# Performance work log

Measured on AMD Instinct MI355X. Metric: run time of the kernel, lower is better.

Reference implementation:

```python
import jax, jax.numpy as jnp
import numpy as np

B = 50000        # mini-batch nodes
NB, M, D = 4, 256, 32   # branches, codebook size, per-branch dim
C = NB * D       # in_channels = out_channels = 128
E = 1000000      # edges per block (intra and cross)
N_GLOBAL = 100000


def setup_inputs() -> dict:
    key = jax.random.key(0)
    ks = jax.random.split(key, 16)
    return {
        "X_B": jax.random.normal(ks[0], (B, C), dtype=jnp.float32),
        "edge_src_bb": jax.random.randint(ks[1], (E,), 0, B),
        "edge_dst_bb": jax.random.randint(ks[2], (E,), 0, B),
        "edge_w_bb": jax.random.uniform(ks[3], (E,), dtype=jnp.float32),
        "edge_src_bm": jax.random.randint(ks[4], (E,), 0, N_GLOBAL),
        "edge_dst_bm": jax.random.randint(ks[5], (E,), 0, B),
        "edge_w_bm": jax.random.uniform(ks[6], (E,), dtype=jnp.float32),
        "c_indices": jax.random.randint(ks[7], (N_GLOBAL,), 0, M),
        "warm_up_rate": jnp.ones((1,), dtype=jnp.float32),
        "codebook": jax.random.normal(ks[8], (NB, M, D), dtype=jnp.float32),
        "vq_grad": jax.random.normal(ks[9], (NB, M, D), dtype=jnp.float32) * 0.01,
        "W_conv": jax.random.normal(ks[10], (NB, D, D), dtype=jnp.float32) / np.sqrt(D),
        "b_conv": jax.random.normal(ks[11], (NB, D), dtype=jnp.float32) * 0.01,
        "W_fc": jax.random.normal(ks[12], (C, C), dtype=jnp.float32) / np.sqrt(C),
        "b_fc": jax.random.normal(ks[13], (C,), dtype=jnp.float32) * 0.01,
    }


def reference(X_B, edge_src_bb, edge_dst_bb, edge_w_bb, edge_src_bm, edge_dst_bm,
              edge_w_bm, c_indices, warm_up_rate, codebook, vq_grad,
              W_conv, b_conv, W_fc, b_fc):
    wr = warm_up_rate[0]
    # split features into NB branches: [NB, B, D]
    Xb = X_B.reshape(B, NB, D).transpose(1, 0, 2)
    # X_input = cat([X_B, codebook * warm_up_rate]) per branch -> [NB, B+M, D]
    X_in = jnp.concatenate([Xb, codebook * wr], axis=1)
    # GCNConv (normalize=False): linear transform then edge-weighted aggregation
    h = jnp.einsum('nbd,nde->nbe', X_in, W_conv)
    # mapper: remap out-of-batch endpoints of cross edges to codeword rows
    src_bm = B + c_indices[edge_src_bm]          # [E] indices into codeword rows
    out = jnp.zeros_like(h)
    # A_BB block: intra-batch message passing
    out = out.at[:, edge_dst_bb].add(edge_w_bb[None, :, None] * h[:, edge_src_bb])
    # A_BM block: batch nodes receive from codewords (quantized neighbors)
    out = out.at[:, edge_dst_bm].add(edge_w_bm[None, :, None] * h[:, src_bm])
    # A_MB block: codeword rows receive from batch nodes (for info_backward)
    out = out.at[:, src_bm].add(edge_w_bm[None, :, None] * h[:, edge_dst_bm])
    out = out + b_conv[:, None, :]
    # info_backward routes approximated gradient through codeword outputs
    info_backward = jnp.sum(out[:, B:] * vq_grad) * wr
    # concat branch outputs for batch nodes, second fc, skip connection
    Xcat = out[:, :B].transpose(1, 0, 2).reshape(B, C)
    Y = Xcat @ W_fc + b_fc + X_B
    return (Y, info_backward)
```

## Files before the change

kernel.cpp:

```cpp
#include <hip/hip_runtime.h>
#include <hip/hip_bf16.h>

#define BN    50000
#define NBR   4
#define MM    256
#define DD    32
#define CC    128
#define EE    1000000
#define ROWS  (BN + MM)
#define NEDGE (2 * EE)
#define SCAN_BLOCKS 49
#define TBITS 13
#define BINS  8
#define NBINS (BN * BINS)
#define SCAN1_BLOCKS 391
#define GBLK  2000
#define GROWS 25

template <int ISBF> struct IO;

template <> struct IO<0> {
    static __device__ float ld(const void* p, long i) { return ((const float*)p)[i]; }
    static __device__ float2 ld2(const void* p, long i) {
        const float* f = (const float*)p + i;
        return make_float2(f[0], f[1]);
    }
    static __device__ void st(void* p, long i, float v) { ((float*)p)[i] = v; }
    static __device__ void st2(void* p, long i, float2 v) {
        float* f = (float*)p + i; f[0] = v.x; f[1] = v.y;
    }
};

template <> struct IO<1> {
    static __device__ float b2f(unsigned short u) {
        return __uint_as_float(((unsigned)u) << 16);
    }
    static __device__ unsigned short f2b(float f) {
        unsigned x = __float_as_uint(f);
        unsigned r = x + 0x7fffu + ((x >> 16) & 1u);
        return (unsigned short)(r >> 16);
    }
    static __device__ float ld(const void* p, long i) {
        return b2f(((const unsigned short*)p)[i]);
    }
    static __device__ float2 ld2(const void* p, long i) {
        unsigned v = *(const unsigned*)((const unsigned short*)p + i);
        return make_float2(b2f((unsigned short)(v & 0xffffu)),
                           b2f((unsigned short)(v >> 16)));
    }
    static __device__ void st(void* p, long i, float v) {
        ((unsigned short*)p)[i] = f2b(v);
    }
    static __device__ void st2(void* p, long i, float2 v) {
        unsigned o = ((unsigned)f2b(v.x)) | (((unsigned)f2b(v.y)) << 16);
        *(unsigned*)((unsigned short*)p + i) = o;
    }
};

template <int ISBF> struct HIO;
template <> struct HIO<0> {
    static __device__ float2 ld(const float* h, long row, int l) {
        return *(const float2*)(h + row * CC + 2 * l);
    }
    static __device__ void st(float* h, long row, int l, float2 v) {
        *(float2*)(h + row * CC + 2 * l) = v;
    }
};
template <> struct HIO<1> {
    static __device__ float2 ld(const float* h, long row, int l) {
        unsigned u = ((const unsigned*)h)[row * (CC / 2) + l];
        return make_float2(IO<1>::b2f((unsigned short)(u & 0xffffu)),
                           IO<1>::b2f((unsigned short)(u >> 16)));
    }
    static __device__ void st(float* h, long row, int l, float2 v) {
        unsigned o = ((unsigned)IO<1>::f2b(v.x)) | (((unsigned)IO<1>::f2b(v.y)) << 16);
        ((unsigned*)h)[row * (CC / 2) + l] = o;
    }
};

static __device__ inline void unpack8(int4 v, float* f) {
    unsigned a = (unsigned)v.x, b = (unsigned)v.y, c = (unsigned)v.z, d = (unsigned)v.w;
    f[0] = IO<1>::b2f((unsigned short)(a & 0xffffu)); f[1] = IO<1>::b2f((unsigned short)(a >> 16));
    f[2] = IO<1>::b2f((unsigned short)(b & 0xffffu)); f[3] = IO<1>::b2f((unsigned short)(b >> 16));
    f[4] = IO<1>::b2f((unsigned short)(c & 0xffffu)); f[5] = IO<1>::b2f((unsigned short)(c >> 16));
    f[6] = IO<1>::b2f((unsigned short)(d & 0xffffu)); f[7] = IO<1>::b2f((unsigned short)(d >> 16));
}
static __device__ inline void fma8(float* acc, float w, int4 v) {
    float f[8]; unpack8(v, f);
#pragma unroll
    for (int k = 0; k < 8; k++) acc[k] += w * f[k];
}
static __device__ inline float dot8(const float* hi, int4 v) {
    float f[8]; unpack8(v, f);
    float s = 0.f;
#pragma unroll
    for (int k = 0; k < 8; k++) s += hi[k] * f[k];
    return s;
}

typedef int iv4 __attribute__((ext_vector_type(4)));
static __device__ inline void nt_store16(void* p, unsigned a, unsigned b,
                                         unsigned c, unsigned d) {
    iv4 x; x[0] = (int)a; x[1] = (int)b; x[2] = (int)c; x[3] = (int)d;
    __builtin_nontemporal_store(x, (iv4*)p);
}

__global__ void kDetect(const void* warm, int* flag) {
    flag[0] = (((const unsigned short*)warm)[0] == 0x3F80u) ? 1 : 0;
}

template <int ISBF>
__device__ void kA_body(const void* X_B, const void* codebook, const void* W_conv,
                        const void* warm, float* __restrict__ hout,
                        float* __restrict__ hcw, float* sW, float* sX) {
    int tid = threadIdx.x;
    int w = tid >> 6, l = tid & 63;
    for (int k = tid; k < NBR * DD * DD; k += 256)
        sW[k] = IO<ISBF>::ld(W_conv, k);
    int r = blockIdx.x * 4 + w;
    int c0 = 2 * l, n = c0 >> 5, e = c0 & 31;
    float2 x2;
    if (r < BN) {
        x2 = IO<ISBF>::ld2(X_B, (long)r * CC + c0);
    } else {
        int m = r - BN;
        float wr = IO<ISBF>::ld(warm, 0);
        x2 = IO<ISBF>::ld2(codebook, (long)n * MM * DD + m * DD + e);
        x2.x *= wr; x2.y *= wr;
    }
    sX[w * CC + c0] = x2.x;
    sX[w * CC + c0 + 1] = x2.y;
    __syncthreads();
    float2 acc = make_float2(0.f, 0.f);
#pragma unroll
    for (int d = 0; d < DD; d++) {
        float xv = sX[w * CC + n * DD + d];
        float2 wv = *(const float2*)&sW[n * DD * DD + d * DD + e];
        acc.x += xv * wv.x;
        acc.y += xv * wv.y;
    }
    if (r < BN) HIO<ISBF>::st(hout, r, l, acc);
    else        HIO<ISBF>::st(hcw, r - BN, l, acc);
}
__global__ __launch_bounds__(256) void kA(const int* flag, const void* X_B,
                                          const void* codebook, const void* W_conv,
                                          const void* warm, float* hout, float* hcw) {
    __shared__ float sW[NBR * DD * DD];
    __shared__ float sX[4 * CC];
    if (*flag) kA_body<1>(X_B, codebook, W_conv, warm, hout, hcw, sW, sX);
    else       kA_body<0>(X_B, codebook, W_conv, warm, hout, hcw, sW, sX);
}

__global__ void kHist(const int* __restrict__ esrc_bb, const int* __restrict__ edst_bb,
                      const int* __restrict__ edst_bm, int* __restrict__ counts) {
    long stride = (long)gridDim.x * blockDim.x;
    for (long i = (long)blockIdx.x * blockDim.x + threadIdx.x; i < NEDGE; i += stride) {
        int bin;
        if (i < EE) bin = (edst_bb[i] << 3) + (esrc_bb[i] >> TBITS);
        else        bin = (edst_bm[i - EE] << 3) + 7;
        atomicAdd(&counts[bin], 1);
    }
}

__global__ __launch_bounds__(1024) void kScan1(const int* __restrict__ counts,
                                               int* __restrict__ offsets,
                                               int* __restrict__ tileSum) {
    __shared__ int s[1024];
    int tid = threadIdx.x;
    int i = blockIdx.x * 1024 + tid;
    int v = (i < NBINS) ? counts[i] : 0;
    s[tid] = v;
    __syncthreads();
    for (int off = 1; off < 1024; off <<= 1) {
        int x = (tid >= off) ? s[tid - off] : 0;
        __syncthreads();
        s[tid] += x;
        __syncthreads();
    }
    if (i < NBINS) offsets[i] = s[tid] - v;
    if (tid == 1023) tileSum[blockIdx.x] = s[tid];
}
__global__ __launch_bounds__(512) void kScan2(int* tileSum) {
    __shared__ int s[512];
    int tid = threadIdx.x;
    int v = (tid < SCAN1_BLOCKS) ? tileSum[tid] : 0;
    s[tid] = v;
    __syncthreads();
    for (int off = 1; off < 512; off <<= 1) {
        int x = (tid >= off) ? s[tid - off] : 0;
        __syncthreads();
        s[tid] += x;
        __syncthreads();
    }
    if (tid < SCAN1_BLOCKS) tileSum[tid] = s[tid] - v;
}
__global__ __launch_bounds__(1024) void kScan3(int* __restrict__ offsets,
                                               const int* __restrict__ tileSum,
                                               int* __restrict__ cursor) {
    int i = blockIdx.x * 1024 + threadIdx.x;
    if (i < NBINS) {
        int o = offsets[i] + tileSum[blockIdx.x];
        offsets[i] = o;
        cursor[i] = o;
    }
    if (blockIdx.x == 0 && threadIdx.x == 0) offsets[NBINS] = NEDGE;
}

template <int ISBF>
__device__ void kFill_body(const int* esrc_bb, const int* edst_bb, const void* ew_bb,
                           const int* esrc_bm, const int* edst_bm, const void* ew_bm,
                           const int* c_idx, int* cursor, int2* entries) {
    long stride = (long)gridDim.x * blockDim.x;
    for (long i = (long)blockIdx.x * blockDim.x + threadIdx.x; i < NEDGE; i += stride) {
        int src, bin; float w;
        if (i < EE) {
            src = esrc_bb[i]; bin = (edst_bb[i] << 3) + (src >> TBITS);
            w = IO<ISBF>::ld(ew_bb, i);
        } else {
            long j = i - EE;
            src = BN + c_idx[esrc_bm[j]]; bin = (edst_bm[j] << 3) + 7;
            w = IO<ISBF>::ld(ew_bm, j);
        }
        int pos = atomicAdd(&cursor[bin], 1);
        long packed = ((long)__float_as_int(w) << 32) | (unsigned)src;
        __builtin_nontemporal_store(packed, (long*)entries + pos);
    }
}
__global__ void kFill(const int* flag, const int* esrc_bb, const int* edst_bb,
                      const void* ew_bb, const int* esrc_bm, const int* edst_bm,
                      const void* ew_bm, const int* c_idx, int* cursor, int2* entries) {
    if (*flag) kFill_body<1>(esrc_bb, edst_bb, ew_bb, esrc_bm, edst_bm, ew_bm, c_idx, cursor, entries);
    else       kFill_body<0>(esrc_bb, edst_bb, ew_bb, esrc_bm, edst_bm, ew_bm, c_idx, cursor, entries);
}

__device__ void kG_body_bf(const unsigned short* __restrict__ hbatch,
                           const unsigned short* __restrict__ hcw,
                           const int2* __restrict__ entries,
                           const int* __restrict__ offsets,
                           const void* b_conv, const void* vq_grad, void* t,
                           float* __restrict__ infoP, float* sAcc) {
    int tid = threadIdx.x;
    for (int k = tid; k < GROWS * CC; k += 256) sAcc[k] = 0.f;
    __syncthreads();
    int l = tid & 63, w = tid >> 6;
    int g = l >> 4;
    int q = l & 15;
    int cb = q * 8;
    int n = cb >> 5, e0 = cb & 31;
    const unsigned short* gb = (const unsigned short*)vq_grad + (long)n * MM * DD + e0;
    int rbase = blockIdx.x * GROWS;

    for (int ph = 0; ph < BINS; ph++) {
        bool bm = (ph == BINS - 1);
        for (int lr = w; lr < GROWS; lr += 4) {
            int r = rbase + lr;
            int bi = (r << 3) + ph;
            int start = __builtin_amdgcn_readfirstlane(offsets[bi]);
            int deg   = __builtin_amdgcn_readfirstlane(offsets[bi + 1]) - start;
            if (deg == 0) continue;
            const long* ep = (const long*)entries + start;
            float acc[8] = {0.f, 0.f, 0.f, 0.f, 0.f, 0.f, 0.f, 0.f};
            float info = 0.f;
            float hi[8];
            if (bm) unpack8(*(const int4*)(hbatch + (long)r * CC + cb), hi);
            for (int j = 0; j < deg; j += 4) {
                int idx = j + g;
                long e8 = __builtin_nontemporal_load(ep + (idx < deg ? idx : 0));
                float wj = (idx < deg) ? __int_as_float((int)(e8 >> 32)) : 0.f;
                int src = (int)(unsigned)(e8 & 0xffffffffL);
                if (!bm) {
                    int4 hv = *(const int4*)(hbatch + (long)src * CC + cb);
                    fma8(acc, wj, hv);
                } else {
                    int m = src - BN;
                    int4 hv = *(const int4*)(hcw + (long)m * CC + cb);
                    fma8(acc, wj, hv);
                    if (wj != 0.f) {
                        int4 gv = *(const int4*)(gb + (long)m * DD);
                        info += wj * dot8(hi, gv);
                    }
                }
            }
#pragma unroll
            for (int k = 0; k < 8; k++) {
                acc[k] += __shfl_xor(acc[k], 16);
                acc[k] += __shfl_xor(acc[k], 32);
            }
            if (g == 0) {
#pragma unroll
                for (int k = 0; k < 8; k++) sAcc[lr * CC + cb + k] += acc[k];
            }
            if (bm) {
                for (int off = 32; off; off >>= 1) info += __shfl_xor(info, off);
                if (l == 0) infoP[r] = info;
            }
        }
        __syncthreads();
    }
    for (int lr = w; lr < GROWS; lr += 4) {
        if (g == 0) {
            int r = rbase + lr;
            float bc[8];
            unpack8(*(const int4*)((const unsigned short*)b_conv + n * DD + e0), bc);
            unsigned o[4];
#pragma unroll
            for (int d = 0; d < 4; d++) {
                float x0 = sAcc[lr * CC + cb + 2 * d]     + bc[2 * d];
                float x1 = sAcc[lr * CC + cb + 2 * d + 1] + bc[2 * d + 1];
                o[d] = ((unsigned)IO<1>::f2b(x0)) | (((unsigned)IO<1>::f2b(x1)) << 16);
            }
            nt_store16((unsigned short*)t + (long)r * CC + cb, o[0], o[1], o[2], o[3]);
        }
    }
}

__device__ void kG_body_f32(const float* __restrict__ hbatch, const float* __restrict__ hcw,
                            const int2* __restrict__ entries,
                            const int* __restrict__ offsets,
                            const void* b_conv, const void* vq_grad, void* t,
                            float* __restrict__ infoP) {
    int tid = threadIdx.x;
    int l = tid & 63;
    int c0 = 2 * l, n = c0 >> 5, e = c0 & 31;
    int wid = (int)((blockIdx.x * blockDim.x + tid) >> 6);
    int nw  = (int)((gridDim.x * blockDim.x) >> 6);
    for (int i = wid; i < BN; i += nw) {
        int start = __builtin_amdgcn_readfirstlane(offsets[i << 3]);
        int deg   = __builtin_amdgcn_readfirstlane(offsets[(i + 1) << 3]) - start;
        const int2* ep = entries + start;
        float2 hi = HIO<0>::ld(hbatch, i, l);
        long gbase = (long)n * MM * DD + e;
        float2 acc = make_float2(0.f, 0.f);
        float info = 0.f;
        for (int j = 0; j < deg; j++) {
            int2 ev = ep[j];
            float wj = __int_as_float(ev.y);
            const float* src = (ev.x < BN) ? (hbatch + (long)ev.x * CC)
                                           : (hcw + (long)(ev.x - BN) * CC);
            float2 hv = *(const float2*)(src + c0);
            acc.x += wj * hv.x;
            acc.y += wj * hv.y;
            if (ev.x >= BN) {
                float2 gv = IO<0>::ld2(vq_grad, gbase + (long)(ev.x - BN) * DD);
                info += wj * (hi.x * gv.x + hi.y * gv.y);
            }
        }
        float2 b2 = IO<0>::ld2(b_conv, n * DD + e);
        IO<0>::st2(t, (long)i * CC + c0, make_float2(acc.x + b2.x, acc.y + b2.y));
        for (int off = 32; off; off >>= 1) info += __shfl_xor(info, off);
        if (l == 0) infoP[i] = info;
    }
}
__global__ __launch_bounds__(256, 8) void kGather(const int* flag, const float* hout,
                                                  const float* hcw, const int2* entries,
                                                  const int* offsets,
                                                  const void* b_conv, const void* vq_grad,
                                                  void* t, float* infoP) {
    __shared__ float sAcc[GROWS * CC];
    if (*flag) kG_body_bf((const unsigned short*)hout, (const unsigned short*)hcw,
                          entries, offsets, b_conv, vq_grad, t, infoP, sAcc);
    else       kG_body_f32(hout, hcw, entries, offsets, b_conv, vq_grad, t, infoP);
}

__global__ __launch_bounds__(1024) void kRed(const float* __restrict__ infoP, float* ibAcc) {
    __shared__ float s[1024];
    int tid = threadIdx.x;
    int i = blockIdx.x * 1024 + tid;
    s[tid] = (i < BN) ? infoP[i] : 0.f;
    __syncthreads();
    for (int st = 512; st; st >>= 1) {
        if (tid < st) s[tid] += s[tid + st];
        __syncthreads();
    }
    if (tid == 0) atomicAdd(ibAcc, s[0]);
}

template <int ISBF>
__device__ void kFC_body(const void* t, const void* W_fc, const void* b_fc,
                         const void* X_B, void* Y, float* sT, float* sW) {
    int tid = threadIdx.x;
    int w = tid >> 6, l = tid & 63;
    int c0 = 2 * l;
    int r0 = blockIdx.x * 32;
    for (int k = tid; k < 32 * CC / 2; k += 512) {
        int row = k >> 6, c = (k & 63) * 2;
        float2 v = make_float2(0.f, 0.f);
        if (r0 + row < BN) v = IO<ISBF>::ld2(t, (long)(r0 + row) * CC + c);
        sT[row * CC + c] = v.x;
        sT[row * CC + c + 1] = v.y;
    }
    float2 y[4];
#pragma unroll
    for (int rr = 0; rr < 4; rr++) y[rr] = make_float2(0.f, 0.f);
    for (int ch = 0; ch < 4; ch++) {
        __syncthreads();
        for (int k = tid; k < 32 * CC / 2; k += 512) {
            int cc = k >> 6, c = (k & 63) * 2;
            float2 v = IO<ISBF>::ld2(W_fc, (long)(ch * 32 + cc) * CC + c);
            sW[cc * CC + c] = v.x;
            sW[cc * CC + c + 1] = v.y;
        }
        __syncthreads();
#pragma unroll 8
        for (int cc = 0; cc < 32; cc++) {
            float2 wv = *(const float2*)&sW[cc * CC + c0];
#pragma unroll
            for (int rr = 0; rr < 4; rr++) {
                float tv = sT[(w * 4 + rr) * CC + ch * 32 + cc];
                y[rr].x += tv * wv.x;
                y[rr].y += tv * wv.y;
            }
        }
    }
    float2 bf = IO<ISBF>::ld2(b_fc, c0);
#pragma unroll
    for (int rr = 0; rr < 4; rr++) {
        int r = r0 + w * 4 + rr;
        if (r < BN) {
            float2 xb = IO<ISBF>::ld2(X_B, (long)r * CC + c0);
            IO<ISBF>::st2(Y, (long)r * CC + c0,
                          make_float2(y[rr].x + bf.x + xb.x, y[rr].y + bf.y + xb.y));
        }
    }
}
__global__ __launch_bounds__(512) void kFC(const int* flag, const void* t, const void* W_fc,
                                           const void* b_fc, const void* X_B, void* Y) {
    __shared__ float sT[32 * CC];
    __shared__ float sW[32 * CC];
    if (*flag) kFC_body<1>(t, W_fc, b_fc, X_B, Y, sT, sW);
    else       kFC_body<0>(t, W_fc, b_fc, X_B, Y, sT, sW);
}

template <int ISBF>
__device__ void kF_body(const void* b_conv, const void* vq_grad, const void* warm,
                        const float* ibAcc, void* out, float* sred) {
    int tid = threadIdx.x;
    float a = 0.f;
    for (int idx = tid; idx < NBR * MM * DD; idx += 256) {
        int nn = idx >> 13, dd = idx & 31;
        a += IO<ISBF>::ld(b_conv, nn * DD + dd) * IO<ISBF>::ld(vq_grad, idx);
    }
    sred[tid] = a;
    __syncthreads();
    for (int s = 128; s; s >>= 1) {
        if (tid < s) sred[tid] += sred[tid + s];
        __syncthreads();
    }
    if (tid == 0) {
        float wr = IO<ISBF>::ld(warm, 0);
        IO<ISBF>::st(out, (long)BN * CC, wr * (ibAcc[0] + sred[0]));
    }
}
__global__ __launch_bounds__(256) void kFinal(const int* flag, const void* b_conv,
                                              const void* vq_grad, const void* warm,
                                              const float* ibAcc, void* out) {
    __shared__ float sred[256];
    if (*flag) kF_body<1>(b_conv, vq_grad, warm, ibAcc, out, sred);
    else       kF_body<0>(b_conv, vq_grad, warm, ibAcc, out, sred);
}

extern "C" void kernel_launch(void* const* d_in, const int* in_sizes, int n_in,
                              void* d_out, int out_size, void* d_ws, size_t ws_size,
                              hipStream_t stream) {
    (void)in_sizes; (void)n_in; (void)out_size;
    const void* X_B      = d_in[0];
    const int*  esrc_bb  = (const int*)d_in[1];
    const int*  edst_bb  = (const int*)d_in[2];
    const void* ew_bb    = d_in[3];
    const int*  esrc_bm  = (const int*)d_in[4];
    const int*  edst_bm  = (const int*)d_in[5];
    const void* ew_bm    = d_in[6];
    const int*  c_idx    = (const int*)d_in[7];
    const void* warm     = d_in[8];
    const void* codebook = d_in[9];
    const void* vq_grad  = d_in[10];
    const void* W_conv   = d_in[11];
    const void* b_conv   = d_in[12];
    const void* W_fc     = d_in[13];
    const void* b_fc     = d_in[14];

    char* ws = (char*)d_ws;
    float* hcw     = (float*)ws;  ws += (size_t)MM * CC * 4;
    float* tbuf    = (float*)ws;  ws += (size_t)BN * CC * 4;
    int2*  entries = (int2*)ws;   ws += (size_t)NEDGE * 8;
    int*   counts  = (int*)ws;    ws += (size_t)NBINS * 4;
    int*   offsets = (int*)ws;    ws += (size_t)(NBINS + 1) * 4;
    int*   cursor  = (int*)ws;    ws += (size_t)NBINS * 4;
    float* infoP   = (float*)ws;  ws += (size_t)BN * 4;
    int*   tileSum = (int*)ws;    ws += 512 * 4;
    float* ibAcc   = (float*)ws;  ws += 16;
    int*   flag    = (int*)ws;    ws += 16;
    if ((size_t)(ws - (char*)d_ws) > ws_size) return;

    float* hout = (float*)d_out;

    hipMemsetAsync(counts, 0, (size_t)NBINS * 4, stream);
    hipMemsetAsync(ibAcc, 0, 4, stream);
    hipMemsetAsync(infoP, 0, (size_t)BN * 4, stream);
    kDetect<<<1, 1, 0, stream>>>(warm, flag);
    kA<<<ROWS / 4, 256, 0, stream>>>(flag, X_B, codebook, W_conv, warm, hout, hcw);
    kHist<<<1024, 256, 0, stream>>>(esrc_bb, edst_bb, edst_bm, counts);
    kScan1<<<SCAN1_BLOCKS, 1024, 0, stream>>>(counts, offsets, tileSum);
    kScan2<<<1, 512, 0, stream>>>(tileSum);
    kScan3<<<SCAN1_BLOCKS, 1024, 0, stream>>>(offsets, tileSum, cursor);
    kFill<<<1024, 256, 0, stream>>>(flag, esrc_bb, edst_bb, ew_bb, esrc_bm, edst_bm,
                                    ew_bm, c_idx, cursor, entries);
    kGather<<<GBLK, 256, 0, stream>>>(flag, hout, hcw, entries, offsets,
                                      b_conv, vq_grad, tbuf, infoP);
    kRed<<<SCAN_BLOCKS, 1024, 0, stream>>>(infoP, ibAcc);
    kFC<<<(BN + 31) / 32, 512, 0, stream>>>(flag, tbuf, W_fc, b_fc, X_B, d_out);
    kFinal<<<1, 256, 0, stream>>>(flag, b_conv, vq_grad, warm, ibAcc, d_out);
}
```

Before: 662.8 us.

## Reorder CSR bins source-tile-major and add grid-wide phase barriers in gather

Changes the bin layout so that bins are grouped by source tile first, then destination, which makes entries of the same source tile contiguous across all destinations. The gather kernel gets a software grid barrier between source-tile phases, so every block works on the same source tile at once and that tile's rows of h stay resident in cache. Block count is halved and rows per block doubled so that all blocks can be co-resident, and launch bounds are relaxed to 6 waves. The barrier relies on all 1000 blocks being resident together; its spin loop has a timeout that prevents a hang if they are not, but block stalls add latency.

```diff
diff --git a/kernel.cpp b/kernel.cpp
--- a/kernel.cpp
+++ b/kernel.cpp
@@ -14,8 +14,8 @@
 #define BINS  8
 #define NBINS (BN * BINS)
 #define SCAN1_BLOCKS 391
-#define GBLK  2000
-#define GROWS 25
+#define GBLK  1000
+#define GROWS 50
 
 template <int ISBF> struct IO;
 
@@ -103,6 +103,20 @@
                                          unsigned c, unsigned d) {
     iv4 x; x[0] = (int)a; x[1] = (int)b; x[2] = (int)c; x[3] = (int)d;
     __builtin_nontemporal_store(x, (iv4*)p);
+}
+
+static __device__ inline void gbar(int* ctr, int ph, int nblk) {
+    __syncthreads();
+    if (threadIdx.x == 0) {
+        __hip_atomic_fetch_add(&ctr[ph], 1, __ATOMIC_ACQ_REL, __HIP_MEMORY_SCOPE_AGENT);
+        int t = 0;
+        while (__hip_atomic_load(&ctr[ph], __ATOMIC_ACQUIRE, __HIP_MEMORY_SCOPE_AGENT) < nblk
+               && t < 40000) {
+            __builtin_amdgcn_s_sleep(8);
+            t++;
+        }
+    }
+    __syncthreads();
 }
 
 __global__ void kDetect(const void* warm, int* flag) {
@@ -156,8 +170,8 @@
     long stride = (long)gridDim.x * blockDim.x;
     for (long i = (long)blockIdx.x * blockDim.x + threadIdx.x; i < NEDGE; i += stride) {
         int bin;
-        if (i < EE) bin = (edst_bb[i] << 3) + (esrc_bb[i] >> TBITS);
-        else        bin = (edst_bm[i - EE] << 3) + 7;
+        if (i < EE) bin = (esrc_bb[i] >> TBITS) * BN + edst_bb[i];
+        else        bin = 7 * BN + edst_bm[i - EE];
         atomicAdd(&counts[bin], 1);
     }
 }
@@ -214,11 +228,11 @@
     for (long i = (long)blockIdx.x * blockDim.x + threadIdx.x; i < NEDGE; i += stride) {
         int src, bin; float w;
         if (i < EE) {
-            src = esrc_bb[i]; bin = (edst_bb[i] << 3) + (src >> TBITS);
+            src = esrc_bb[i]; bin = (src >> TBITS) * BN + edst_bb[i];
             w = IO<ISBF>::ld(ew_bb, i);
         } else {
             long j = i - EE;
-            src = BN + c_idx[esrc_bm[j]]; bin = (edst_bm[j] << 3) + 7;
+            src = BN + c_idx[esrc_bm[j]]; bin = 7 * BN + edst_bm[j];
             w = IO<ISBF>::ld(ew_bm, j);
         }
         int pos = atomicAdd(&cursor[bin], 1);
@@ -238,7 +252,7 @@
                            const int2* __restrict__ entries,
                            const int* __restrict__ offsets,
                            const void* b_conv, const void* vq_grad, void* t,
-                           float* __restrict__ infoP, float* sAcc) {
+                           float* __restrict__ infoP, int* pcnt, float* sAcc) {
     int tid = threadIdx.x;
     for (int k = tid; k < GROWS * CC; k += 256) sAcc[k] = 0.f;
     __syncthreads();
@@ -254,7 +268,7 @@
         bool bm = (ph == BINS - 1);
         for (int lr = w; lr < GROWS; lr += 4) {
             int r = rbase + lr;
-            int bi = (r << 3) + ph;
+            int bi = ph * BN + r;
             int start = __builtin_amdgcn_readfirstlane(offsets[bi]);
             int deg   = __builtin_amdgcn_readfirstlane(offsets[bi + 1]) - start;
             if (deg == 0) continue;
@@ -295,7 +309,7 @@
                 if (l == 0) infoP[r] = info;
             }
         }
-        __syncthreads();
+        if (ph <= BINS - 3) gbar(pcnt, ph, GBLK);
     }
     for (int lr = w; lr < GROWS; lr += 4) {
         if (g == 0) {
@@ -325,24 +339,27 @@
     int wid = (int)((blockIdx.x * blockDim.x + tid) >> 6);
     int nw  = (int)((gridDim.x * blockDim.x) >> 6);
     for (int i = wid; i < BN; i += nw) {
-        int start = __builtin_amdgcn_readfirstlane(offsets[i << 3]);
-        int deg   = __builtin_amdgcn_readfirstlane(offsets[(i + 1) << 3]) - start;
-        const int2* ep = entries + start;
         float2 hi = HIO<0>::ld(hbatch, i, l);
         long gbase = (long)n * MM * DD + e;
         float2 acc = make_float2(0.f, 0.f);
         float info = 0.f;
-        for (int j = 0; j < deg; j++) {
-            int2 ev = ep[j];
-            float wj = __int_as_float(ev.y);
-            const float* src = (ev.x < BN) ? (hbatch + (long)ev.x * CC)
-                                           : (hcw + (long)(ev.x - BN) * CC);
-            float2 hv = *(const float2*)(src + c0);
-            acc.x += wj * hv.x;
-            acc.y += wj * hv.y;
-            if (ev.x >= BN) {
-                float2 gv = IO<0>::ld2(vq_grad, gbase + (long)(ev.x - BN) * DD);
-                info += wj * (hi.x * gv.x + hi.y * gv.y);
+        for (int ph = 0; ph < BINS; ph++) {
+            int bi = ph * BN + i;
+            int start = __builtin_amdgcn_readfirstlane(offsets[bi]);
+            int deg   = __builtin_amdgcn_readfirstlane(offsets[bi + 1]) - start;
+            const int2* ep = entries + start;
+            for (int j = 0; j < deg; j++) {
+                int2 ev = ep[j];
+                float wj = __int_as_float(ev.y);
+                const float* src = (ev.x < BN) ? (hbatch + (long)ev.x * CC)
+                                               : (hcw + (long)(ev.x - BN) * CC);
+                float2 hv = *(const float2*)(src + c0);
+                acc.x += wj * hv.x;
+                acc.y += wj * hv.y;
+                if (ev.x >= BN) {
+                    float2 gv = IO<0>::ld2(vq_grad, gbase + (long)(ev.x - BN) * DD);
+                    info += wj * (hi.x * gv.x + hi.y * gv.y);
+                }
             }
         }
         float2 b2 = IO<0>::ld2(b_conv, n * DD + e);
@@ -351,14 +368,14 @@
         if (l == 0) infoP[i] = info;
     }
 }
-__global__ __launch_bounds__(256, 8) void kGather(const int* flag, const float* hout,
+__global__ __launch_bounds__(256, 6) void kGather(const int* flag, const float* hout,
                                                   const float* hcw, const int2* entries,
                                                   const int* offsets,
                                                   const void* b_conv, const void* vq_grad,
-                                                  void* t, float* infoP) {
+                                                  void* t, float* infoP, int* pcnt) {
     __shared__ float sAcc[GROWS * CC];
     if (*flag) kG_body_bf((const unsigned short*)hout, (const unsigned short*)hcw,
-                          entries, offsets, b_conv, vq_grad, t, infoP, sAcc);
+                          entries, offsets, b_conv, vq_grad, t, infoP, pcnt, sAcc);
     else       kG_body_f32(hout, hcw, entries, offsets, b_conv, vq_grad, t, infoP);
 }
 
@@ -488,6 +505,7 @@
     int*   cursor  = (int*)ws;    ws += (size_t)NBINS * 4;
     float* infoP   = (float*)ws;  ws += (size_t)BN * 4;
     int*   tileSum = (int*)ws;    ws += 512 * 4;
+    int*   phaseCtr= (int*)ws;    ws += 16 * 4;
     float* ibAcc   = (float*)ws;  ws += 16;
     int*   flag    = (int*)ws;    ws += 16;
     if ((size_t)(ws - (char*)d_ws) > ws_size) return;
@@ -497,6 +515,7 @@
     hipMemsetAsync(counts, 0, (size_t)NBINS * 4, stream);
     hipMemsetAsync(ibAcc, 0, 4, stream);
     hipMemsetAsync(infoP, 0, (size_t)BN * 4, stream);
+    hipMemsetAsync(phaseCtr, 0, 16 * 4, stream);
     kDetect<<<1, 1, 0, stream>>>(warm, flag);
     kA<<<ROWS / 4, 256, 0, stream>>>(flag, X_B, codebook, W_conv, warm, hout, hcw);
     kHist<<<1024, 256, 0, stream>>>(esrc_bb, edst_bb, edst_bm, counts);
@@ -506,7 +525,7 @@
     kFill<<<1024, 256, 0, stream>>>(flag, esrc_bb, edst_bb, ew_bb, esrc_bm, edst_bm,
                                     ew_bm, c_idx, cursor, entries);
     kGather<<<GBLK, 256, 0, stream>>>(flag, hout, hcw, entries, offsets,
-                                      b_conv, vq_grad, tbuf, infoP);
+                                      b_conv, vq_grad, tbuf, infoP, phaseCtr);
     kRed<<<SCAN_BLOCKS, 1024, 0, stream>>>(infoP, ibAcc);
     kFC<<<(BN + 31) / 32, 512, 0, stream>>>(flag, tbuf, W_fc, b_fc, X_B, d_out);
     kFinal<<<1, 256, 0, stream>>>(flag, b_conv, vq_grad, warm, ibAcc, d_out);
```

Measured after the change: 826.3 us. 24.7% more time.
